# Kernel tuning notes

Measured on AMD Instinct MI355X. Metric: run time of the kernel, lower is better.

## Reference

```python
import jax, jax.numpy as jnp
from jax import lax
import numpy as np

VOCAB, EMBED, HID, MAXLEN, BATCH = 50000, 512, 1024, 100, 512
FORGET_BIAS = 2.0


def setup_inputs() -> dict:
    key = jax.random.key(0)
    ks = jax.random.split(key, 12)
    s = 0.02
    input_queries = jax.random.randint(ks[0], (BATCH, MAXLEN), 0, VOCAB, dtype=jnp.int32)
    input_replies = jax.random.randint(ks[1], (BATCH, MAXLEN), 0, VOCAB, dtype=jnp.int32)
    query_lengths = jnp.maximum(jax.random.randint(ks[2], (BATCH,), 0, MAXLEN, dtype=jnp.int32), 1)
    reply_lengths = jnp.maximum(jax.random.randint(ks[3], (BATCH,), 0, MAXLEN, dtype=jnp.int32), 1)
    embeddings = jax.random.normal(ks[4], (VOCAB, EMBED), dtype=jnp.float32) * s
    # shared peephole LSTM weights (reuse=True in the original): kernel over [x; h], gate order i, j, f, o
    W = jax.random.normal(ks[5], (EMBED + HID, 4 * HID), dtype=jnp.float32) * s
    b = jnp.zeros((4 * HID,), dtype=jnp.float32)
    p_i = jax.random.normal(ks[6], (HID,), dtype=jnp.float32) * s
    p_f = jax.random.normal(ks[7], (HID,), dtype=jnp.float32) * s
    p_o = jax.random.normal(ks[8], (HID,), dtype=jnp.float32) * s
    M = jax.random.normal(ks[9], (HID, HID), dtype=jnp.float32) * s
    return {
        "embeddings": embeddings, "W": W, "b": b,
        "p_i": p_i, "p_f": p_f, "p_o": p_o, "M": M,
        "input_queries": input_queries, "input_replies": input_replies,
        "query_lengths": query_lengths, "reply_lengths": reply_lengths,
    }


def _lstm_encode(x_emb, lengths, W, b, p_i, p_f, p_o):
    """Peephole LSTM (TF LSTMCell, use_peepholes=True). Returns final h at sequence_length."""
    B, L, _ = x_emb.shape
    H = p_i.shape[0]

    def step(carry, xt):
        c, h = carry
        x_t, t = xt                      # x_t: [B, E]
        z = jnp.concatenate([x_t, h], axis=-1) @ W + b   # [B, 4H]
        zi, zj, zf, zo = jnp.split(z, 4, axis=-1)
        i = jax.nn.sigmoid(zi + p_i * c)
        f = jax.nn.sigmoid(zf + FORGET_BIAS + p_f * c)
        c_new = f * c + i * jnp.tanh(zj)
        o = jax.nn.sigmoid(zo + p_o * c_new)
        h_new = o * jnp.tanh(c_new)
        valid = (t < lengths)[:, None]   # hold state past sequence_length
        return (jnp.where(valid, c_new, c), jnp.where(valid, h_new, h)), None

    init = (jnp.zeros((B, H), x_emb.dtype), jnp.zeros((B, H), x_emb.dtype))
    xs = (jnp.swapaxes(x_emb, 0, 1), jnp.arange(L, dtype=jnp.int32))
    (_, h), _ = lax.scan(step, init, xs)
    return h


def reference(embeddings, W, b, p_i, p_f, p_o, M,
              input_queries, input_replies, query_lengths, reply_lengths):
    q_emb = embeddings[input_queries]    # [B, L, E]
    r_emb = embeddings[input_replies]
    q_enc = _lstm_encode(q_emb, query_lengths, W, b, p_i, p_f, p_o)   # [B, H]
    r_enc = _lstm_encode(r_emb, reply_lengths, W, b, p_i, p_f, p_o)
    q_t = q_enc @ M                                                    # bilinear transform
    distances = q_t @ r_enc.T                                          # [B, B]
    # positives = diagonal, negatives = all off-diagonal (in-batch negatives)
    labels = jnp.eye(distances.shape[0], dtype=distances.dtype)
    # sigmoid cross entropy: softplus(x) - label * x, mean over all B*B logits
    loss = jnp.mean(jax.nn.softplus(distances) - labels * distances)
    return distances, loss
```

## Files before the change

### kernel.cpp

```cpp
#include <hip/hip_runtime.h>
#include <stdint.h>

typedef unsigned short u16;
typedef __bf16 bf16x8 __attribute__((ext_vector_type(8)));
typedef float f32x4 __attribute__((ext_vector_type(4)));

#define AS1 __attribute__((address_space(1)))
#define AS3 __attribute__((address_space(3)))

__device__ __forceinline__ void ld_lds16(const void* gp, void* lp) {
  __builtin_amdgcn_global_load_lds((AS1 void*)(void*)gp, (AS3 void*)lp, 16, 0, 0);
}

__device__ __forceinline__ u16 f2bf(float f) {
  uint32_t u = __float_as_uint(f);
  u += 0x7FFFu + ((u >> 16) & 1u);
  return (u16)(u >> 16);
}

__device__ __forceinline__ float fsig(float x) { return 1.0f / (1.0f + __expf(-x)); }
__device__ __forceinline__ float ftanhf(float x) {
  float e = __expf(-2.0f * fabsf(x));
  float t = (1.0f - e) / (1.0f + e);
  return copysignf(t, x);
}

#define LSEQ 100
#define EMB 512
#define HID 1024
#define KDIM 1536

__global__ __launch_bounds__(512, 2) void k_step(
    const u16* __restrict__ emb, const u16* __restrict__ W2T,
    const float* __restrict__ b2, const float* __restrict__ p_i,
    const float* __restrict__ p_f, const float* __restrict__ p_o,
    const int* __restrict__ tokQ, const int* __restrict__ tokR,
    const int* __restrict__ lenQ, const int* __restrict__ lenR,
    const u16* __restrict__ h_cur, u16* __restrict__ h_nxt,
    float* __restrict__ c_st, int t)
{
  __shared__ u16 sb[4 * 16384];
  const int tid = threadIdx.x;
  const int lane = tid & 63, wid = tid >> 6;
  const int wm = wid >> 1, wn = wid & 1;
  const int lane_lo = lane & 15, lane_hi = lane >> 4;
  const int g = blockIdx.x;
  const int bx = (g & 7) * 4 + ((g >> 3) & 3);
  const int by = g >> 5;

  f32x4 acc[2][4];
  const f32x4 zz = {0.f, 0.f, 0.f, 0.f};
#pragma unroll
  for (int a = 0; a < 2; ++a)
#pragma unroll
    for (int bb = 0; bb < 4; ++bb) acc[a][bb] = zz;

  int tokv[2], rowe[2], rowi[2], ldso[2], srco[2];
#pragma unroll
  for (int j = 0; j < 2; ++j) {
    const int cbase = (j * 8 + wid) * 64;
    const int ch = cbase + lane;
    const int r = ch >> 3;
    const int srcoff = ((((ch & 7) << 4) ^ ((r & 7) << 4)) >> 1);
    const int m = by * 128 + r, e = m >> 9, i = m & 511;
    tokv[j] = (e ? tokR : tokQ)[i * LSEQ + t];
    rowe[j] = e; rowi[j] = i;
    srco[j] = srcoff;
    ldso[j] = cbase * 8;
  }

  const int colbase = bx * 128 + wn * 64;
  const int h = ((colbase >> 6) << 4) + lane_lo;
  float b2v[4];
#pragma unroll
  for (int gg = 0; gg < 4; ++gg) b2v[gg] = b2[colbase + gg * 16 + lane_lo];
  const float pi = p_i[h], pf = p_f[h], po = p_o[h];
  int lenv[2][4];
  float cold[2][4];
  u16 hprev[2][4];
#pragma unroll
  for (int mi = 0; mi < 2; ++mi)
#pragma unroll
    for (int r = 0; r < 4; ++r) {
      const int m = by * 128 + wm * 32 + mi * 16 + lane_hi * 4 + r;
      const int e = m >> 9, i = m & 511;
      lenv[mi][r] = e ? lenR[i] : lenQ[i];
      const size_t ci = (size_t)(e * 512 + i) * HID + h;
      cold[mi][r] = c_st[ci];
      hprev[mi][r] = h_cur[ci];
    }
  __builtin_amdgcn_sched_barrier(0);

  const u16* pAx[2];
  const u16* pAh[2];
  const u16* pB[2];
#pragma unroll
  for (int j = 0; j < 2; ++j) {
    const int cbase = (j * 8 + wid) * 64;
    const int r = (cbase + lane) >> 3;
    pAx[j] = emb + (size_t)tokv[j] * EMB + srco[j];
    pAh[j] = h_cur + (size_t)(rowe[j] * 512 + rowi[j]) * HID - 512 + srco[j];
    pB[j]  = W2T + (size_t)(bx * 128 + r) * KDIM + srco[j];
  }

  auto stage = [&](int kt, int buf) {
    const int kb = kt * 64;
    u16* lA = sb + buf * 16384;
    u16* lB = lA + 8192;
    const bool isx = kb < EMB;
#pragma unroll
    for (int j = 0; j < 2; ++j) ld_lds16((isx ? pAx[j] : pAh[j]) + kb, lA + ldso[j]);
#pragma unroll
    for (int j = 0; j < 2; ++j) ld_lds16(pB[j] + kb, lB + ldso[j]);
  };

  auto compute = [&](int buf) {
    const u16* lA = sb + buf * 16384;
    const u16* lB = lA + 8192;
#pragma unroll
    for (int kk = 0; kk < 2; ++kk) {
      bf16x8 aF[2], bF[4];
#pragma unroll
      for (int mi = 0; mi < 2; ++mi) {
        const int rr = wm * 32 + mi * 16 + lane_lo;
        const int byo = rr * 128 + ((kk * 64 + lane_hi * 16) ^ ((rr & 7) << 4));
        aF[mi] = *(const bf16x8*)((const char*)lA + byo);
      }
#pragma unroll
      for (int ni = 0; ni < 4; ++ni) {
        const int rr = wn * 64 + ni * 16 + lane_lo;
        const int byo = rr * 128 + ((kk * 64 + lane_hi * 16) ^ ((rr & 7) << 4));
        bF[ni] = *(const bf16x8*)((const char*)lB + byo);
      }
#pragma unroll
      for (int mi = 0; mi < 2; ++mi)
#pragma unroll
        for (int ni = 0; ni < 4; ++ni)
          acc[mi][ni] = __builtin_amdgcn_mfma_f32_16x16x32_bf16(aF[mi], bF[ni], acc[mi][ni], 0, 0, 0);
    }
  };

  stage(0, 0);
  stage(1, 1);
  stage(2, 2);

  for (int kt = 0; kt < 24; ++kt) {
    if (kt <= 21)      asm volatile("s_waitcnt vmcnt(8)" ::: "memory");
    else if (kt == 22) asm volatile("s_waitcnt vmcnt(4)" ::: "memory");
    else               asm volatile("s_waitcnt vmcnt(0)" ::: "memory");
    __builtin_amdgcn_s_barrier();
    __builtin_amdgcn_sched_barrier(0);
    if (kt < 21) stage(kt + 3, (kt + 3) & 3);
    __builtin_amdgcn_s_setprio(1);
    compute(kt & 3);
    __builtin_amdgcn_s_setprio(0);
  }

#pragma unroll
  for (int mi = 0; mi < 2; ++mi) {
#pragma unroll
    for (int r = 0; r < 4; ++r) {
      const int m = by * 128 + wm * 32 + mi * 16 + lane_hi * 4 + r;
      const int e = m >> 9, i = m & 511;
      const size_t ci = (size_t)(e * 512 + i) * HID + h;
      u16 hv;
      if (t < lenv[mi][r]) {
        const float c_old = cold[mi][r];
        const float zi = acc[mi][0][r] + b2v[0] + pi * c_old;
        const float zj = acc[mi][1][r] + b2v[1];
        const float zf = acc[mi][2][r] + b2v[2] + pf * c_old;
        const float zo = acc[mi][3][r] + b2v[3];
        const float ig = fsig(zi), fg = fsig(zf);
        const float cn = fg * c_old + ig * ftanhf(zj);
        const float og = fsig(zo + po * cn);
        const float hn = og * ftanhf(cn);
        c_st[ci] = cn;
        hv = f2bf(hn);
      } else {
        hv = hprev[mi][r];
      }
      h_nxt[ci] = hv;
    }
  }
}

template <int OUT_BF16>
__global__ __launch_bounds__(256) void k_gemm(
    const u16* __restrict__ A, const u16* __restrict__ Bn,
    void* __restrict__ Cout, int K, int ldc)
{
  __shared__ u16 lA[128 * 64];
  __shared__ u16 lB[128 * 64];
  const int tid = threadIdx.x;
  const int lane = tid & 63, wid = tid >> 6;
  const int wm = wid >> 1, wn = wid & 1;
  const int lane_lo = lane & 15, lane_hi = lane >> 4;
  const int bx = blockIdx.x, by = blockIdx.y;

  f32x4 acc[4][4];
  const f32x4 zz = {0.f, 0.f, 0.f, 0.f};
#pragma unroll
  for (int a = 0; a < 4; ++a)
#pragma unroll
    for (int bb = 0; bb < 4; ++bb) acc[a][bb] = zz;

  const int nkt = K >> 6;
  for (int kt = 0; kt < nkt; ++kt) {
    const int kb = kt * 64;
#pragma unroll
    for (int j = 0; j < 4; ++j) {
      const int cbase = (j * 4 + wid) * 64;
      const int ch = cbase + lane;
      const int r = ch >> 3;
      const int srcoff = ((((ch & 7) << 4) ^ ((r & 7) << 4)) >> 1);
      ld_lds16(A + (size_t)(by * 128 + r) * K + kb + srcoff, &lA[cbase * 8]);
    }
#pragma unroll
    for (int j = 0; j < 4; ++j) {
      const int cbase = (j * 4 + wid) * 64;
      const int ch = cbase + lane;
      const int r = ch >> 3;
      const int srcoff = ((((ch & 7) << 4) ^ ((r & 7) << 4)) >> 1);
      ld_lds16(Bn + (size_t)(bx * 128 + r) * K + kb + srcoff, &lB[cbase * 8]);
    }
    __syncthreads();
#pragma unroll
    for (int kk = 0; kk < 2; ++kk) {
      bf16x8 aF[4], bF[4];
#pragma unroll
      for (int mi = 0; mi < 4; ++mi) {
        const int rr = wm * 64 + mi * 16 + lane_lo;
        const int byo = rr * 128 + ((kk * 64 + lane_hi * 16) ^ ((rr & 7) << 4));
        aF[mi] = *(const bf16x8*)((const char*)lA + byo);
      }
#pragma unroll
      for (int ni = 0; ni < 4; ++ni) {
        const int rr = wn * 64 + ni * 16 + lane_lo;
        const int byo = rr * 128 + ((kk * 64 + lane_hi * 16) ^ ((rr & 7) << 4));
        bF[ni] = *(const bf16x8*)((const char*)lB + byo);
      }
#pragma unroll
      for (int mi = 0; mi < 4; ++mi)
#pragma unroll
        for (int ni = 0; ni < 4; ++ni)
          acc[mi][ni] = __builtin_amdgcn_mfma_f32_16x16x32_bf16(aF[mi], bF[ni], acc[mi][ni], 0, 0, 0);
    }
    __syncthreads();
  }

#pragma unroll
  for (int mi = 0; mi < 4; ++mi)
#pragma unroll
    for (int r = 0; r < 4; ++r) {
      const int m = by * 128 + wm * 64 + mi * 16 + lane_hi * 4 + r;
#pragma unroll
      for (int ni = 0; ni < 4; ++ni) {
        const int col = bx * 128 + wn * 64 + ni * 16 + lane_lo;
        const float v = acc[mi][ni][r];
        if (OUT_BF16) ((u16*)Cout)[(size_t)m * ldc + col] = f2bf(v);
        else ((float*)Cout)[(size_t)m * ldc + col] = v;
      }
    }
}

__global__ void k_transpose(const float* __restrict__ in, u16* __restrict__ out,
                            int K_, int N_, int perm)
{
  __shared__ float tile[64][65];
  const int tid = threadIdx.x;
  const int k0 = blockIdx.y * 64, n0 = blockIdx.x * 64;
  const int c = tid & 63, rq = tid >> 6;
  for (int rr = 0; rr < 64; rr += 4)
    tile[rr + rq][c] = in[(size_t)(k0 + rr + rq) * N_ + n0 + c];
  __syncthreads();
  for (int nr0 = 0; nr0 < 64; nr0 += 4) {
    const int nr = nr0 + rq;
    const int n = n0 + nr;
    int np = n;
    if (perm) {
      const int g = n >> 10, hh = n & 1023;
      np = ((hh >> 4) << 6) + (g << 4) + (hh & 15);
    }
    out[(size_t)np * K_ + k0 + c] = f2bf(tile[c][nr]);
  }
}

__global__ void k_bias(const float* __restrict__ b, float* __restrict__ b2) {
  const int n = blockIdx.x * 256 + threadIdx.x;
  if (n < 4096) {
    const int g = n >> 10, hh = n & 1023;
    const int np = ((hh >> 4) << 6) + (g << 4) + (hh & 15);
    b2[np] = b[n] + (g == 2 ? 2.0f : 0.0f);
  }
}

__global__ void k_cvt(const float4* __restrict__ in, u16* __restrict__ out, size_t n4) {
  size_t idx = (size_t)blockIdx.x * blockDim.x + threadIdx.x;
  const size_t stride = (size_t)gridDim.x * blockDim.x;
  for (; idx < n4; idx += stride) {
    const float4 v = in[idx];
    ushort4 o;
    o.x = f2bf(v.x); o.y = f2bf(v.y); o.z = f2bf(v.z); o.w = f2bf(v.w);
    *(ushort4*)(out + idx * 4) = o;
  }
}

__global__ void k_zero(uint4* __restrict__ p, size_t n) {
  size_t idx = (size_t)blockIdx.x * blockDim.x + threadIdx.x;
  const size_t stride = (size_t)gridDim.x * blockDim.x;
  const uint4 z = {0u, 0u, 0u, 0u};
  for (; idx < n; idx += stride) p[idx] = z;
}

__global__ void k_loss1(const float* __restrict__ D, float* __restrict__ part) {
  __shared__ float sd[256];
  const int tid = threadIdx.x;
  float s = 0.f;
  for (int idx = blockIdx.x * 256 + tid; idx < 512 * 512; idx += 256 * 256) {
    const float x = D[idx];
    float sp;
    if (x > 20.f) sp = x;
    else if (x < -20.f) sp = __expf(x);
    else sp = __logf(1.0f + __expf(x));
    if ((idx >> 9) == (idx & 511)) sp -= x;
    s += sp;
  }
  sd[tid] = s;
  __syncthreads();
  for (int o = 128; o > 0; o >>= 1) { if (tid < o) sd[tid] += sd[tid + o]; __syncthreads(); }
  if (tid == 0) part[blockIdx.x] = sd[0];
}

__global__ void k_loss2(const float* __restrict__ part, float* __restrict__ out) {
  __shared__ float sd[256];
  const int tid = threadIdx.x;
  sd[tid] = part[tid];
  __syncthreads();
  for (int o = 128; o > 0; o >>= 1) { if (tid < o) sd[tid] += sd[tid + o]; __syncthreads(); }
  if (tid == 0) out[0] = sd[0] * (1.0f / (512.0f * 512.0f));
}

extern "C" void kernel_launch(void* const* d_in, const int* in_sizes, int n_in,
                              void* d_out, int out_size, void* d_ws, size_t ws_size,
                              hipStream_t stream)
{
  const float* embF = (const float*)d_in[0];
  const float* W    = (const float*)d_in[1];
  const float* b    = (const float*)d_in[2];
  const float* p_i  = (const float*)d_in[3];
  const float* p_f  = (const float*)d_in[4];
  const float* p_o  = (const float*)d_in[5];
  const float* Mm   = (const float*)d_in[6];
  const int* tokQ   = (const int*)d_in[7];
  const int* tokR   = (const int*)d_in[8];
  const int* lenQ   = (const int*)d_in[9];
  const int* lenR   = (const int*)d_in[10];
  float* out = (float*)d_out;

  char* ws = (char*)d_ws;
  const size_t OFF_EMB  = 0;
  const size_t OFF_W2T  = 51200000;
  const size_t OFF_MT   = OFF_W2T + 12582912;
  const size_t OFF_B2   = OFF_MT + 2097152;
  const size_t OFF_H    = OFF_B2 + 16384;
  const size_t OFF_C    = OFF_H + 4194304;
  const size_t OFF_QT   = OFF_C + 4194304;
  const size_t OFF_PART = OFF_QT + 1048576;
  const size_t NEED = OFF_PART + 1024;
  if (ws_size < NEED) return;

  u16* embB  = (u16*)(ws + OFF_EMB);
  u16* W2T   = (u16*)(ws + OFF_W2T);
  u16* MT    = (u16*)(ws + OFF_MT);
  float* b2  = (float*)(ws + OFF_B2);
  u16* hbuf  = (u16*)(ws + OFF_H);
  float* cst = (float*)(ws + OFF_C);
  u16* qt    = (u16*)(ws + OFF_QT);
  float* part= (float*)(ws + OFF_PART);

  k_cvt<<<dim3(2048), dim3(256), 0, stream>>>((const float4*)embF, embB, (size_t)(50000 * 512 / 4));
  k_transpose<<<dim3(64, 24), dim3(256), 0, stream>>>(W, W2T, 1536, 4096, 1);
  k_transpose<<<dim3(16, 16), dim3(256), 0, stream>>>(Mm, MT, 1024, 1024, 0);
  k_bias<<<dim3(16), dim3(256), 0, stream>>>(b, b2);
  k_zero<<<dim3(256), dim3(256), 0, stream>>>((uint4*)hbuf, 131072);
  k_zero<<<dim3(256), dim3(256), 0, stream>>>((uint4*)cst, 262144);

  const size_t HBUFSTRIDE = (size_t)2 * 512 * 1024;
  for (int t = 0; t < 100; ++t) {
    u16* hc = hbuf + (size_t)(t & 1) * HBUFSTRIDE;
    u16* hn = hbuf + (size_t)((t + 1) & 1) * HBUFSTRIDE;
    k_step<<<dim3(256), dim3(512), 0, stream>>>(embB, W2T, b2, p_i, p_f, p_o,
                                                tokQ, tokR, lenQ, lenR, hc, hn, cst, t);
  }

  k_gemm<1><<<dim3(8, 4), dim3(256), 0, stream>>>(hbuf, MT, qt, 1024, 1024);
  k_gemm<0><<<dim3(4, 4), dim3(256), 0, stream>>>(qt, hbuf + (size_t)512 * 1024, out, 1024, 512);

  k_loss1<<<dim3(256), dim3(256), 0, stream>>>(out, part);
  k_loss2<<<dim3(1), dim3(256), 0, stream>>>(part, out + 262144);
}
```

Baseline: 2.061 ms.

## Shrink LSTM step tile to 64x128 with 512 blocks and triple buffering

The per-timestep gate GEMM kernel now uses 256-thread blocks that each own a 64-row M tile instead of 128, doubling the grid to 512 blocks so more of the GPU's compute units are busy. The LDS pipeline drops from four buffers with three stages in flight to three buffers with two in flight, and the load offsets and waitcnt values are recomputed to match. Each block loads the same W tile for half as many rows, so W bandwidth per FLOP goes up and prefetch depth goes down.

```diff
diff --git a/kernel.cpp b/kernel.cpp
--- a/kernel.cpp
+++ b/kernel.cpp
@@ -30,7 +30,7 @@
 #define HID 1024
 #define KDIM 1536
 
-__global__ __launch_bounds__(512, 2) void k_step(
+__global__ __launch_bounds__(256, 2) void k_step(
     const u16* __restrict__ emb, const u16* __restrict__ W2T,
     const float* __restrict__ b2, const float* __restrict__ p_i,
     const float* __restrict__ p_f, const float* __restrict__ p_o,
@@ -39,7 +39,7 @@
     const u16* __restrict__ h_cur, u16* __restrict__ h_nxt,
     float* __restrict__ c_st, int t)
 {
-  __shared__ u16 sb[4 * 16384];
+  __shared__ u16 sb[3 * 12288];
   const int tid = threadIdx.x;
   const int lane = tid & 63, wid = tid >> 6;
   const int wm = wid >> 1, wn = wid & 1;
@@ -55,18 +55,17 @@
 #pragma unroll
     for (int bb = 0; bb < 4; ++bb) acc[a][bb] = zz;
 
-  int tokv[2], rowe[2], rowi[2], ldso[2], srco[2];
+  int tokv[2], rowe[2], rowi[2], ldsoA[2], srcoA[2];
 #pragma unroll
   for (int j = 0; j < 2; ++j) {
-    const int cbase = (j * 8 + wid) * 64;
-    const int ch = cbase + lane;
+    const int ch = j * 256 + tid;
     const int r = ch >> 3;
-    const int srcoff = ((((ch & 7) << 4) ^ ((r & 7) << 4)) >> 1);
-    const int m = by * 128 + r, e = m >> 9, i = m & 511;
+    const int srcoff = ((ch & 7) ^ (r & 7)) * 8;
+    const int m = by * 64 + r, e = m >> 9, i = m & 511;
     tokv[j] = (e ? tokR : tokQ)[i * LSEQ + t];
     rowe[j] = e; rowi[j] = i;
-    srco[j] = srcoff;
-    ldso[j] = cbase * 8;
+    srcoA[j] = srcoff;
+    ldsoA[j] = ch * 8;
   }
 
   const int colbase = bx * 128 + wn * 64;
@@ -82,7 +81,7 @@
   for (int mi = 0; mi < 2; ++mi)
 #pragma unroll
     for (int r = 0; r < 4; ++r) {
-      const int m = by * 128 + wm * 32 + mi * 16 + lane_hi * 4 + r;
+      const int m = by * 64 + wm * 32 + mi * 16 + lane_hi * 4 + r;
       const int e = m >> 9, i = m & 511;
       lenv[mi][r] = e ? lenR[i] : lenQ[i];
       const size_t ci = (size_t)(e * 512 + i) * HID + h;
@@ -93,30 +92,36 @@
 
   const u16* pAx[2];
   const u16* pAh[2];
-  const u16* pB[2];
+  const u16* pB[4];
+  int ldsoB[4];
 #pragma unroll
   for (int j = 0; j < 2; ++j) {
-    const int cbase = (j * 8 + wid) * 64;
-    const int r = (cbase + lane) >> 3;
-    pAx[j] = emb + (size_t)tokv[j] * EMB + srco[j];
-    pAh[j] = h_cur + (size_t)(rowe[j] * 512 + rowi[j]) * HID - 512 + srco[j];
-    pB[j]  = W2T + (size_t)(bx * 128 + r) * KDIM + srco[j];
+    pAx[j] = emb + (size_t)tokv[j] * EMB + srcoA[j];
+    pAh[j] = h_cur + (size_t)(rowe[j] * 512 + rowi[j]) * HID - 512 + srcoA[j];
+  }
+#pragma unroll
+  for (int j = 0; j < 4; ++j) {
+    const int ch = j * 256 + tid;
+    const int r = ch >> 3;
+    const int srcoff = ((ch & 7) ^ (r & 7)) * 8;
+    pB[j] = W2T + (size_t)(bx * 128 + r) * KDIM + srcoff;
+    ldsoB[j] = ch * 8;
   }
 
   auto stage = [&](int kt, int buf) {
     const int kb = kt * 64;
-    u16* lA = sb + buf * 16384;
-    u16* lB = lA + 8192;
+    u16* lA = sb + buf * 12288;
+    u16* lB = lA + 4096;
     const bool isx = kb < EMB;
 #pragma unroll
-    for (int j = 0; j < 2; ++j) ld_lds16((isx ? pAx[j] : pAh[j]) + kb, lA + ldso[j]);
-#pragma unroll
-    for (int j = 0; j < 2; ++j) ld_lds16(pB[j] + kb, lB + ldso[j]);
+    for (int j = 0; j < 2; ++j) ld_lds16((isx ? pAx[j] : pAh[j]) + kb, lA + ldsoA[j]);
+#pragma unroll
+    for (int j = 0; j < 4; ++j) ld_lds16(pB[j] + kb, lB + ldsoB[j]);
   };
 
   auto compute = [&](int buf) {
-    const u16* lA = sb + buf * 16384;
-    const u16* lB = lA + 8192;
+    const u16* lA = sb + buf * 12288;
+    const u16* lB = lA + 4096;
 #pragma unroll
     for (int kk = 0; kk < 2; ++kk) {
       bf16x8 aF[2], bF[4];
@@ -142,17 +147,15 @@
 
   stage(0, 0);
   stage(1, 1);
-  stage(2, 2);
 
   for (int kt = 0; kt < 24; ++kt) {
-    if (kt <= 21)      asm volatile("s_waitcnt vmcnt(8)" ::: "memory");
-    else if (kt == 22) asm volatile("s_waitcnt vmcnt(4)" ::: "memory");
-    else               asm volatile("s_waitcnt vmcnt(0)" ::: "memory");
+    if (kt < 23) asm volatile("s_waitcnt vmcnt(6)" ::: "memory");
+    else         asm volatile("s_waitcnt vmcnt(0)" ::: "memory");
     __builtin_amdgcn_s_barrier();
     __builtin_amdgcn_sched_barrier(0);
-    if (kt < 21) stage(kt + 3, (kt + 3) & 3);
+    if (kt < 22) stage(kt + 2, (kt + 2) % 3);
     __builtin_amdgcn_s_setprio(1);
-    compute(kt & 3);
+    compute(kt % 3);
     __builtin_amdgcn_s_setprio(0);
   }
 
@@ -160,7 +163,7 @@
   for (int mi = 0; mi < 2; ++mi) {
 #pragma unroll
     for (int r = 0; r < 4; ++r) {
-      const int m = by * 128 + wm * 32 + mi * 16 + lane_hi * 4 + r;
+      const int m = by * 64 + wm * 32 + mi * 16 + lane_hi * 4 + r;
       const int e = m >> 9, i = m & 511;
       const size_t ci = (size_t)(e * 512 + i) * HID + h;
       u16 hv;
@@ -389,7 +392,7 @@
   for (int t = 0; t < 100; ++t) {
     u16* hc = hbuf + (size_t)(t & 1) * HBUFSTRIDE;
     u16* hn = hbuf + (size_t)((t + 1) & 1) * HBUFSTRIDE;
-    k_step<<<dim3(256), dim3(512), 0, stream>>>(embB, W2T, b2, p_i, p_f, p_o,
+    k_step<<<dim3(512), dim3(256), 0, stream>>>(embB, W2T, b2, p_i, p_f, p_o,
                                                 tokQ, tokR, lenQ, lenR, hc, hn, cst, t);
   }
 
```

Measured after the change: 2.098 ms (median of 2 runs). About the same (+1.8%).

## Fuse LSTM timesteps into one persistent cooperative kernel with grid sync

Applied to the files above, without the earlier changes.

Replaces the 100 per-timestep launches with a single cooperative kernel that loops over timesteps and separates them with grid.sync(). The cell state now stays in registers instead of being read from and written to global memory each step. The embedding and weight tiles for the next step's first K-blocks are prefetched before the grid barrier. Held-past-length rows are copied only once, at t == len. This trades launch overhead and c-state traffic for grid-wide barrier cost, and it needs every block to be co-resident on the GPU.

```diff
diff --git a/kernel.cpp b/kernel.cpp
--- a/kernel.cpp
+++ b/kernel.cpp
@@ -1,5 +1,8 @@
 #include <hip/hip_runtime.h>
+#include <hip/hip_cooperative_groups.h>
 #include <stdint.h>
+
+namespace cg = cooperative_groups;
 
 typedef unsigned short u16;
 typedef __bf16 bf16x8 __attribute__((ext_vector_type(8)));
@@ -30,15 +33,15 @@
 #define HID 1024
 #define KDIM 1536
 
-__global__ __launch_bounds__(512, 2) void k_step(
+__global__ __launch_bounds__(512, 2) void k_lstm(
     const u16* __restrict__ emb, const u16* __restrict__ W2T,
     const float* __restrict__ b2, const float* __restrict__ p_i,
     const float* __restrict__ p_f, const float* __restrict__ p_o,
     const int* __restrict__ tokQ, const int* __restrict__ tokR,
     const int* __restrict__ lenQ, const int* __restrict__ lenR,
-    const u16* __restrict__ h_cur, u16* __restrict__ h_nxt,
-    float* __restrict__ c_st, int t)
+    u16* __restrict__ h0, u16* __restrict__ h1)
 {
+  cg::grid_group grid = cg::this_grid();
   __shared__ u16 sb[4 * 16384];
   const int tid = threadIdx.x;
   const int lane = tid & 63, wid = tid >> 6;
@@ -48,25 +51,29 @@
   const int bx = (g & 7) * 4 + ((g >> 3) & 3);
   const int by = g >> 5;
 
-  f32x4 acc[2][4];
-  const f32x4 zz = {0.f, 0.f, 0.f, 0.f};
-#pragma unroll
-  for (int a = 0; a < 2; ++a)
-#pragma unroll
-    for (int bb = 0; bb < 4; ++bb) acc[a][bb] = zz;
-
-  int tokv[2], rowe[2], rowi[2], ldso[2], srco[2];
+  int ldsoA[2], srcoA[2];
+  long long rowAoff[2];
+  const int* tokptr[2];
 #pragma unroll
   for (int j = 0; j < 2; ++j) {
-    const int cbase = (j * 8 + wid) * 64;
-    const int ch = cbase + lane;
+    const int ch = j * 512 + tid;
     const int r = ch >> 3;
-    const int srcoff = ((((ch & 7) << 4) ^ ((r & 7) << 4)) >> 1);
+    const int srcoff = ((ch & 7) ^ (r & 7)) * 8;
     const int m = by * 128 + r, e = m >> 9, i = m & 511;
-    tokv[j] = (e ? tokR : tokQ)[i * LSEQ + t];
-    rowe[j] = e; rowi[j] = i;
-    srco[j] = srcoff;
-    ldso[j] = cbase * 8;
+    tokptr[j] = (e ? tokR : tokQ) + i * LSEQ;
+    rowAoff[j] = (long long)(e * 512 + i) * HID - 512 + srcoff;
+    srcoA[j] = srcoff;
+    ldsoA[j] = ch * 8;
+  }
+  const u16* pB[2];
+  int ldsoB[2];
+#pragma unroll
+  for (int j = 0; j < 2; ++j) {
+    const int ch = j * 512 + tid;
+    const int r = ch >> 3;
+    const int srcoff = ((ch & 7) ^ (r & 7)) * 8;
+    pB[j] = W2T + (size_t)(bx * 128 + r) * KDIM + srcoff;
+    ldsoB[j] = ch * 8;
   }
 
   const int colbase = bx * 128 + wn * 64;
@@ -76,8 +83,8 @@
   for (int gg = 0; gg < 4; ++gg) b2v[gg] = b2[colbase + gg * 16 + lane_lo];
   const float pi = p_i[h], pf = p_f[h], po = p_o[h];
   int lenv[2][4];
-  float cold[2][4];
-  u16 hprev[2][4];
+  uint32_t cio[2][4];
+  float creg[2][4];
 #pragma unroll
   for (int mi = 0; mi < 2; ++mi)
 #pragma unroll
@@ -85,35 +92,29 @@
       const int m = by * 128 + wm * 32 + mi * 16 + lane_hi * 4 + r;
       const int e = m >> 9, i = m & 511;
       lenv[mi][r] = e ? lenR[i] : lenQ[i];
-      const size_t ci = (size_t)(e * 512 + i) * HID + h;
-      cold[mi][r] = c_st[ci];
-      hprev[mi][r] = h_cur[ci];
-    }
-  __builtin_amdgcn_sched_barrier(0);
-
+      cio[mi][r] = (uint32_t)((e * 512 + i) * HID + h);
+      creg[mi][r] = 0.f;
+    }
+
+  const u16* hb[2] = {h0, h1};
   const u16* pAx[2];
-  const u16* pAh[2];
-  const u16* pB[2];
-#pragma unroll
-  for (int j = 0; j < 2; ++j) {
-    const int cbase = (j * 8 + wid) * 64;
-    const int r = (cbase + lane) >> 3;
-    pAx[j] = emb + (size_t)tokv[j] * EMB + srco[j];
-    pAh[j] = h_cur + (size_t)(rowe[j] * 512 + rowi[j]) * HID - 512 + srco[j];
-    pB[j]  = W2T + (size_t)(bx * 128 + r) * KDIM + srco[j];
-  }
-
-  auto stage = [&](int kt, int buf) {
+
+  auto stage = [&](int kt, const u16* hcur) {
     const int kb = kt * 64;
-    u16* lA = sb + buf * 16384;
+    u16* lA = sb + (kt & 3) * 16384;
     u16* lB = lA + 8192;
-    const bool isx = kb < EMB;
-#pragma unroll
-    for (int j = 0; j < 2; ++j) ld_lds16((isx ? pAx[j] : pAh[j]) + kb, lA + ldso[j]);
-#pragma unroll
-    for (int j = 0; j < 2; ++j) ld_lds16(pB[j] + kb, lB + ldso[j]);
+    if (kb < EMB) {
+#pragma unroll
+      for (int j = 0; j < 2; ++j) ld_lds16(pAx[j] + kb, lA + ldsoA[j]);
+    } else {
+#pragma unroll
+      for (int j = 0; j < 2; ++j) ld_lds16(hcur + rowAoff[j] + kb, lA + ldsoA[j]);
+    }
+#pragma unroll
+    for (int j = 0; j < 2; ++j) ld_lds16(pB[j] + kb, lB + ldsoB[j]);
   };
 
+  f32x4 acc[2][4];
   auto compute = [&](int buf) {
     const u16* lA = sb + buf * 16384;
     const u16* lB = lA + 8192;
@@ -140,46 +141,66 @@
     }
   };
 
-  stage(0, 0);
-  stage(1, 1);
-  stage(2, 2);
-
-  for (int kt = 0; kt < 24; ++kt) {
-    if (kt <= 21)      asm volatile("s_waitcnt vmcnt(8)" ::: "memory");
-    else if (kt == 22) asm volatile("s_waitcnt vmcnt(4)" ::: "memory");
-    else               asm volatile("s_waitcnt vmcnt(0)" ::: "memory");
-    __builtin_amdgcn_s_barrier();
-    __builtin_amdgcn_sched_barrier(0);
-    if (kt < 21) stage(kt + 3, (kt + 3) & 3);
-    __builtin_amdgcn_s_setprio(1);
-    compute(kt & 3);
-    __builtin_amdgcn_s_setprio(0);
-  }
-
-#pragma unroll
-  for (int mi = 0; mi < 2; ++mi) {
-#pragma unroll
-    for (int r = 0; r < 4; ++r) {
-      const int m = by * 128 + wm * 32 + mi * 16 + lane_hi * 4 + r;
-      const int e = m >> 9, i = m & 511;
-      const size_t ci = (size_t)(e * 512 + i) * HID + h;
-      u16 hv;
-      if (t < lenv[mi][r]) {
-        const float c_old = cold[mi][r];
-        const float zi = acc[mi][0][r] + b2v[0] + pi * c_old;
-        const float zj = acc[mi][1][r] + b2v[1];
-        const float zf = acc[mi][2][r] + b2v[2] + pf * c_old;
-        const float zo = acc[mi][3][r] + b2v[3];
-        const float ig = fsig(zi), fg = fsig(zf);
-        const float cn = fg * c_old + ig * ftanhf(zj);
-        const float og = fsig(zo + po * cn);
-        const float hn = og * ftanhf(cn);
-        c_st[ci] = cn;
-        hv = f2bf(hn);
-      } else {
-        hv = hprev[mi][r];
-      }
-      h_nxt[ci] = hv;
+  {
+    int tk0 = tokptr[0][0], tk1 = tokptr[1][0];
+    pAx[0] = emb + (size_t)tk0 * EMB + srcoA[0];
+    pAx[1] = emb + (size_t)tk1 * EMB + srcoA[1];
+    stage(0, h0); stage(1, h0); stage(2, h0);
+  }
+
+  for (int t = 0; t < 100; ++t) {
+    const u16* hcur = hb[t & 1];
+    u16* hnxt = (u16*)hb[(t + 1) & 1];
+    const f32x4 zz = {0.f, 0.f, 0.f, 0.f};
+#pragma unroll
+    for (int a = 0; a < 2; ++a)
+#pragma unroll
+      for (int bb = 0; bb < 4; ++bb) acc[a][bb] = zz;
+
+    for (int kt = 0; kt < 24; ++kt) {
+      if (kt < 22)       asm volatile("s_waitcnt vmcnt(8)" ::: "memory");
+      else if (kt == 22) asm volatile("s_waitcnt vmcnt(4)" ::: "memory");
+      else               asm volatile("s_waitcnt vmcnt(0)" ::: "memory");
+      __builtin_amdgcn_s_barrier();
+      __builtin_amdgcn_sched_barrier(0);
+      if (kt < 21) stage(kt + 3, hcur);
+      __builtin_amdgcn_s_setprio(1);
+      compute(kt & 3);
+      __builtin_amdgcn_s_setprio(0);
+    }
+
+    int tk0 = 0, tk1 = 0;
+    if (t < 99) { tk0 = tokptr[0][t + 1]; tk1 = tokptr[1][t + 1]; }
+
+#pragma unroll
+    for (int mi = 0; mi < 2; ++mi) {
+#pragma unroll
+      for (int r = 0; r < 4; ++r) {
+        const int len = lenv[mi][r];
+        const uint32_t ci = cio[mi][r];
+        if (t < len) {
+          const float c_old = creg[mi][r];
+          const float zi = acc[mi][0][r] + b2v[0] + pi * c_old;
+          const float zj = acc[mi][1][r] + b2v[1];
+          const float zf = acc[mi][2][r] + b2v[2] + pf * c_old;
+          const float zo = acc[mi][3][r] + b2v[3];
+          const float ig = fsig(zi), fg = fsig(zf);
+          const float cn = fg * c_old + ig * ftanhf(zj);
+          const float og = fsig(zo + po * cn);
+          const float hn = og * ftanhf(cn);
+          creg[mi][r] = cn;
+          hnxt[ci] = f2bf(hn);
+        } else if (t == len) {
+          hnxt[ci] = hcur[ci];
+        }
+      }
+    }
+
+    if (t < 99) {
+      pAx[0] = emb + (size_t)tk0 * EMB + srcoA[0];
+      pAx[1] = emb + (size_t)tk1 * EMB + srcoA[1];
+      stage(0, hcur); stage(1, hcur); stage(2, hcur);
+      grid.sync();
     }
   }
 }
@@ -363,8 +384,7 @@
   const size_t OFF_MT   = OFF_W2T + 12582912;
   const size_t OFF_B2   = OFF_MT + 2097152;
   const size_t OFF_H    = OFF_B2 + 16384;
-  const size_t OFF_C    = OFF_H + 4194304;
-  const size_t OFF_QT   = OFF_C + 4194304;
+  const size_t OFF_QT   = OFF_H + 4194304;
   const size_t OFF_PART = OFF_QT + 1048576;
   const size_t NEED = OFF_PART + 1024;
   if (ws_size < NEED) return;
@@ -374,7 +394,6 @@
   u16* MT    = (u16*)(ws + OFF_MT);
   float* b2  = (float*)(ws + OFF_B2);
   u16* hbuf  = (u16*)(ws + OFF_H);
-  float* cst = (float*)(ws + OFF_C);
   u16* qt    = (u16*)(ws + OFF_QT);
   float* part= (float*)(ws + OFF_PART);
 
@@ -383,14 +402,18 @@
   k_transpose<<<dim3(16, 16), dim3(256), 0, stream>>>(Mm, MT, 1024, 1024, 0);
   k_bias<<<dim3(16), dim3(256), 0, stream>>>(b, b2);
   k_zero<<<dim3(256), dim3(256), 0, stream>>>((uint4*)hbuf, 131072);
-  k_zero<<<dim3(256), dim3(256), 0, stream>>>((uint4*)cst, 262144);
-
-  const size_t HBUFSTRIDE = (size_t)2 * 512 * 1024;
-  for (int t = 0; t < 100; ++t) {
-    u16* hc = hbuf + (size_t)(t & 1) * HBUFSTRIDE;
-    u16* hn = hbuf + (size_t)((t + 1) & 1) * HBUFSTRIDE;
-    k_step<<<dim3(256), dim3(512), 0, stream>>>(embB, W2T, b2, p_i, p_f, p_o,
-                                                tokQ, tokR, lenQ, lenR, hc, hn, cst, t);
+
+  {
+    u16* h0 = hbuf;
+    u16* h1 = hbuf + (size_t)2 * 512 * 1024;
+    const u16* embB_c = embB; const u16* W2T_c = W2T; const float* b2_c = b2;
+    void* kargs[] = {
+      (void*)&embB_c, (void*)&W2T_c, (void*)&b2_c,
+      (void*)&p_i, (void*)&p_f, (void*)&p_o,
+      (void*)&tokQ, (void*)&tokR, (void*)&lenQ, (void*)&lenR,
+      (void*)&h0, (void*)&h1
+    };
+    hipLaunchCooperativeKernel((void*)k_lstm, dim3(256), dim3(512), kargs, 0, stream);
   }
 
   k_gemm<1><<<dim3(8, 4), dim3(256), 0, stream>>>(hbuf, MT, qt, 1024, 1024);
```

Result: slower. 4.434 ms (median of 2 runs) (+115.1%).
